# Kernel tuning notes

Measured on AMD Instinct MI355X. Metric: run time of the kernel, lower is better.

Reference implementation:

```python
import jax, jax.numpy as jnp
import numpy as np

D, DFF, H = 768, 3072, 12
HD = D // H
EPS = 1e-12

def _ln(t, gamma, beta):
    mu = t.mean(-1, keepdims=True)
    var = jnp.mean((t - mu) ** 2, -1, keepdims=True)
    return gamma * (t - mu) / jnp.sqrt(var + EPS) + beta

def setup_inputs() -> dict:
    key = jax.random.key(0)
    ks = jax.random.split(key, 16)
    s = 0.02
    x = jax.random.normal(ks[0], (2, 2048, D), jnp.float32)
    mask = jnp.ones((2, 2048), jnp.float32)
    def lin(k, out_d, in_d):
        kw, kb = jax.random.split(k)
        return (jax.random.normal(kw, (out_d, in_d), jnp.float32) * s,
                jnp.zeros((out_d,), jnp.float32))
    Wq, bq = lin(ks[1], D, D)
    Wk, bk = lin(ks[2], D, D)
    Wv, bv = lin(ks[3], D, D)
    Wp, bp = lin(ks[4], D, D)
    W1, bf1 = lin(ks[5], DFF, D)
    W2, bf2 = lin(ks[6], D, DFF)
    g1 = jnp.ones((D,), jnp.float32); be1 = jnp.zeros((D,), jnp.float32)
    g2 = jnp.ones((D,), jnp.float32); be2 = jnp.zeros((D,), jnp.float32)
    return dict(x=x, mask=mask, Wq=Wq, bq=bq, Wk=Wk, bk=bk, Wv=Wv, bv=bv,
                Wp=Wp, bp=bp, g1=g1, be1=be1, W1=W1, bf1=bf1, W2=W2, bf2=bf2,
                g2=g2, be2=be2)

def reference(x, mask, Wq, bq, Wk, bk, Wv, bv, Wp, bp, g1, be1, W1, bf1, W2, bf2, g2, be2):
    B, S, _ = x.shape
    # projections (torch Linear: x @ W^T + b)
    q = (x @ Wq.T + bq).reshape(B, S, H, HD).transpose(0, 2, 1, 3)  # [B,H,S,HD]
    k = (x @ Wk.T + bk).reshape(B, S, H, HD).transpose(0, 2, 1, 3)
    v = (x @ Wv.T + bv).reshape(B, S, H, HD).transpose(0, 2, 1, 3)
    scores = jnp.einsum('bhqd,bhkd->bhqk', q, k) / jnp.sqrt(jnp.float32(HD))
    scores = scores - 10000.0 * (1.0 - mask[:, None, None, :])
    p = jax.nn.softmax(scores, axis=-1)  # dropout is identity at eval
    h = jnp.einsum('bhqk,bhkd->bqhd', p, v).reshape(B, S, D)
    h = h @ Wp.T + bp
    x1 = _ln(x + h, g1, be1)
    ff = jax.nn.gelu(x1 @ W1.T + bf1, approximate=False) @ W2.T + bf2
    return _ln(x1 + ff, g2, be2)
```

## Files before the change

### kernel.cpp

```cpp
#include <hip/hip_runtime.h>
#include <hip/hip_bf16.h>
#include <math.h>

#define D_MODEL 768
#define D_FF    3072
#define N_HEAD  12
#define HEAD_D  64
#define BATCH   2
#define SEQ     2048
#define QKV_LD  2304

typedef __attribute__((ext_vector_type(8))) short short8;
typedef __attribute__((ext_vector_type(8))) unsigned short ushort8;
typedef __attribute__((ext_vector_type(4))) float f32x4;

__device__ inline unsigned short f2bf(float f) {
    union { __hip_bfloat16 b; unsigned short u; } cv;
    cv.b = __float2bfloat16(f);
    return cv.u;
}

__device__ inline float bf2f(unsigned short u) {
    union { unsigned int i; float f; } cv;
    cv.i = ((unsigned int)u) << 16;
    return cv.f;
}

__device__ inline void async_load16(const void* g, void* l) {
    __builtin_amdgcn_global_load_lds(
        (const __attribute__((address_space(1))) void*)g,
        (__attribute__((address_space(3))) void*)l, 16, 0, 0);
}

__global__ __launch_bounds__(256) void conv_fused(
    const float* __restrict__ x,
    const float* __restrict__ Wq, const float* __restrict__ Wk,
    const float* __restrict__ Wv, const float* __restrict__ Wp,
    const float* __restrict__ W1, const float* __restrict__ W2,
    const float* __restrict__ bq, const float* __restrict__ bk,
    const float* __restrict__ bv,
    unsigned short* __restrict__ xb, unsigned short* __restrict__ wqkvb,
    unsigned short* __restrict__ wpb, unsigned short* __restrict__ w1b,
    unsigned short* __restrict__ w2b, float* __restrict__ bqkv)
{
    int bid = blockIdx.x;
    const float* src; unsigned short* dst; int base;
    if      (bid < 3072) { src = x;  dst = xb;              base = bid;        }
    else if (bid < 3648) { src = Wq; dst = wqkvb;           base = bid - 3072; }
    else if (bid < 4224) { src = Wk; dst = wqkvb + 589824;  base = bid - 3648; }
    else if (bid < 4800) { src = Wv; dst = wqkvb + 1179648; base = bid - 4224; }
    else if (bid < 5376) { src = Wp; dst = wpb;             base = bid - 4800; }
    else if (bid < 7680) { src = W1; dst = w1b;             base = bid - 5376; }
    else if (bid < 9984) { src = W2; dst = w2b;             base = bid - 7680; }
    else {
        for (int j = threadIdx.x; j < QKV_LD; j += 256)
            bqkv[j] = (j < 768) ? bq[j] : (j < 1536) ? bk[j - 768] : bv[j - 1536];
        return;
    }
    int i = (base * 256 + threadIdx.x) * 4;
    float4 v = *(const float4*)(src + i);
    ushort4 o4;
    o4.x = f2bf(v.x); o4.y = f2bf(v.y); o4.z = f2bf(v.z); o4.w = f2bf(v.w);
    *(ushort4*)(dst + i) = o4;
}

#define NSTAGE 3

__global__ __launch_bounds__(256) void gemm_bf16(
    const unsigned short* __restrict__ A, int lda,
    const unsigned short* __restrict__ W, int ldw,
    const float* __restrict__ bias,
    const unsigned short* __restrict__ resb, int ldr,
    float* __restrict__ outf, unsigned short* __restrict__ outb,
    float* __restrict__ pacc, int ldo,
    int M, int N, int K, int mode)
{
    __shared__ unsigned short As[NSTAGE][128 * 32];
    __shared__ unsigned short Bs[NSTAGE][128 * 32];

    const int t    = threadIdx.x;
    const int lane = t & 63;
    const int wv   = t >> 6;
    const int wm   = wv >> 1;
    const int wn   = wv & 1;
    const int bm   = blockIdx.y * 128;
    const int bn   = blockIdx.x * 128;
    const int kz   = blockIdx.z;
    const int Kc   = K / gridDim.z;

    const int qd   = lane >> 4;
    const int l16  = lane & 15;

    f32x4 acc[4][4];
    #pragma unroll
    for (int i = 0; i < 4; i++)
        #pragma unroll
        for (int j = 0; j < 4; j++)
            acc[i][j] = (f32x4){0.f, 0.f, 0.f, 0.f};

    const int srow = lane >> 2;
    const int sseg = (lane & 3) * 8;
    const int r0   = (wv * 2 + 0) * 16 + srow;
    const int r1   = (wv * 2 + 1) * 16 + srow;
    const size_t gA0 = (size_t)(bm + r0) * lda + sseg;
    const size_t gA1 = (size_t)(bm + r1) * lda + sseg;
    const size_t gB0 = (size_t)(bn + r0) * ldw + sseg;
    const size_t gB1 = (size_t)(bn + r1) * ldw + sseg;
    const int c0 = (wv * 2 + 0) * 512;
    const int c1 = (wv * 2 + 1) * 512;

    const int kbeg  = kz * Kc;
    const int niter = Kc / 32;

    async_load16(A + gA0 + kbeg, &As[0][c0]);
    async_load16(W + gB0 + kbeg, &Bs[0][c0]);
    async_load16(A + gA1 + kbeg, &As[0][c1]);
    async_load16(W + gB1 + kbeg, &Bs[0][c1]);
    if (niter > 1) {
        async_load16(A + gA0 + kbeg + 32, &As[1][c0]);
        async_load16(W + gB0 + kbeg + 32, &Bs[1][c0]);
        async_load16(A + gA1 + kbeg + 32, &As[1][c1]);
        async_load16(W + gB1 + kbeg + 32, &Bs[1][c1]);
    }

    int stage = 0;
    for (int it = 0; it < niter; it++) {
        if (it + 1 < niter) __builtin_amdgcn_s_waitcnt(0x0F74);
        else                __builtin_amdgcn_s_waitcnt(0x0F70);
        __builtin_amdgcn_s_barrier();

        if (it + 2 < niter) {
            const int sn = (stage + 2 >= NSTAGE) ? stage + 2 - NSTAGE : stage + 2;
            const int kn = kbeg + (it + 2) * 32;
            async_load16(A + gA0 + kn, &As[sn][c0]);
            async_load16(W + gB0 + kn, &Bs[sn][c0]);
            async_load16(A + gA1 + kn, &As[sn][c1]);
            async_load16(W + gB1 + kn, &Bs[sn][c1]);
        }

        short8 af[4], bf[4];
        #pragma unroll
        for (int mt = 0; mt < 4; mt++)
            af[mt] = *(const short8*)(&As[stage][(wm * 64 + mt * 16 + l16) * 32 + qd * 8]);
        #pragma unroll
        for (int nt = 0; nt < 4; nt++)
            bf[nt] = *(const short8*)(&Bs[stage][(wn * 64 + nt * 16 + l16) * 32 + qd * 8]);
        #pragma unroll
        for (int mt = 0; mt < 4; mt++)
            #pragma unroll
            for (int nt = 0; nt < 4; nt++)
                acc[mt][nt] = __builtin_amdgcn_mfma_f32_16x16x32_bf16(
                    af[mt], bf[nt], acc[mt][nt], 0, 0, 0);

        stage = (stage == NSTAGE - 1) ? 0 : stage + 1;
    }

    #pragma unroll
    for (int mt = 0; mt < 4; mt++) {
        #pragma unroll
        for (int nt = 0; nt < 4; nt++) {
            int col = bn + wn * 64 + nt * 16 + l16;
            float bv = (kz == 0) ? bias[col] : 0.f;
            #pragma unroll
            for (int r = 0; r < 4; r++) {
                int row = bm + wm * 64 + mt * 16 + qd * 4 + r;
                if (kz != 0) {
                    pacc[(size_t)row * ldo + col] = acc[mt][nt][r];
                    continue;
                }
                float v = acc[mt][nt][r] + bv;
                if (mode == 1) {
                    v += bf2f(resb[(size_t)row * ldr + col]);
                    outf[(size_t)row * ldo + col] = v;
                } else if (mode == 2) {
                    v = 0.5f * v * (1.0f + erff(v * 0.70710678118654752f));
                    outb[(size_t)row * ldo + col] = f2bf(v);
                } else if (mode == 3) {
                    outb[(size_t)row * ldo + col] = f2bf(v);
                } else {
                    outf[(size_t)row * ldo + col] = v;
                }
            }
        }
    }
}

__global__ __launch_bounds__(256) void gemm_qkv(
    const unsigned short* __restrict__ A,
    const unsigned short* __restrict__ W,
    const float* __restrict__ bias,
    unsigned short* __restrict__ outb)
{
    __shared__ unsigned short As[4][128 * 32];
    __shared__ unsigned short Bs[4][128 * 32];

    const int t    = threadIdx.x;
    const int lane = t & 63;
    const int wv   = t >> 6;
    const int wm   = wv >> 1;
    const int wn   = wv & 1;

    const int flat = blockIdx.y * 18 + blockIdx.x;
    const int xcd  = flat & 7;
    const int u    = flat >> 3;
    const int mi   = (xcd >> 1) * 8 + u / 9;
    const int ni   = (xcd & 1) * 9 + u % 9;
    const int bm   = mi * 128;
    const int bn   = ni * 128;

    const int qd   = lane >> 4;
    const int l16  = lane & 15;

    f32x4 acc[4][4];
    #pragma unroll
    for (int i = 0; i < 4; i++)
        #pragma unroll
        for (int j = 0; j < 4; j++)
            acc[i][j] = (f32x4){0.f, 0.f, 0.f, 0.f};

    const int srow = lane >> 2;
    const int sseg = (lane & 3) * 8;
    const int r0   = (wv * 2 + 0) * 16 + srow;
    const int r1   = (wv * 2 + 1) * 16 + srow;
    const size_t gA0 = (size_t)(bm + r0) * D_MODEL + sseg;
    const size_t gA1 = (size_t)(bm + r1) * D_MODEL + sseg;
    const size_t gB0 = (size_t)(bn + r0) * D_MODEL + sseg;
    const size_t gB1 = (size_t)(bn + r1) * D_MODEL + sseg;
    const int c0 = (wv * 2 + 0) * 512;
    const int c1 = (wv * 2 + 1) * 512;

    const int niter = D_MODEL / 32;

    async_load16(A + gA0, &As[0][c0]);
    async_load16(W + gB0, &Bs[0][c0]);
    async_load16(A + gA1, &As[0][c1]);
    async_load16(W + gB1, &Bs[0][c1]);
    async_load16(A + gA0 + 32, &As[1][c0]);
    async_load16(W + gB0 + 32, &Bs[1][c0]);
    async_load16(A + gA1 + 32, &As[1][c1]);
    async_load16(W + gB1 + 32, &Bs[1][c1]);
    async_load16(A + gA0 + 64, &As[2][c0]);
    async_load16(W + gB0 + 64, &Bs[2][c0]);
    async_load16(A + gA1 + 64, &As[2][c1]);
    async_load16(W + gB1 + 64, &Bs[2][c1]);

    int stage = 0;
    for (int it = 0; it < niter; it++) {
        if      (it + 2 < niter) __builtin_amdgcn_s_waitcnt(0x0F78);
        else if (it + 1 < niter) __builtin_amdgcn_s_waitcnt(0x0F74);
        else                     __builtin_amdgcn_s_waitcnt(0x0F70);
        __builtin_amdgcn_s_barrier();

        if (it + 3 < niter) {
            int sn = stage + 3;
            if (sn >= 4) sn -= 4;
            const int kn = (it + 3) * 32;
            async_load16(A + gA0 + kn, &As[sn][c0]);
            async_load16(W + gB0 + kn, &Bs[sn][c0]);
            async_load16(A + gA1 + kn, &As[sn][c1]);
            async_load16(W + gB1 + kn, &Bs[sn][c1]);
        }

        short8 af[4], bf[4];
        #pragma unroll
        for (int mt = 0; mt < 4; mt++)
            af[mt] = *(const short8*)(&As[stage][(wm * 64 + mt * 16 + l16) * 32 + qd * 8]);
        #pragma unroll
        for (int nt = 0; nt < 4; nt++)
            bf[nt] = *(const short8*)(&Bs[stage][(wn * 64 + nt * 16 + l16) * 32 + qd * 8]);
        #pragma unroll
        for (int mt = 0; mt < 4; mt++)
            #pragma unroll
            for (int nt = 0; nt < 4; nt++)
                acc[mt][nt] = __builtin_amdgcn_mfma_f32_16x16x32_bf16(
                    af[mt], bf[nt], acc[mt][nt], 0, 0, 0);

        stage = (stage == 3) ? 0 : stage + 1;
    }

    #pragma unroll
    for (int mt = 0; mt < 4; mt++) {
        #pragma unroll
        for (int nt = 0; nt < 4; nt++) {
            int col = bn + wn * 64 + nt * 16 + l16;
            float bv = bias[col];
            #pragma unroll
            for (int r = 0; r < 4; r++) {
                int row = bm + wm * 64 + mt * 16 + qd * 4 + r;
                outb[(size_t)row * QKV_LD + col] = f2bf(acc[mt][nt][r] + bv);
            }
        }
    }
}

__global__ __launch_bounds__(256) void gemm_ffn1(
    const unsigned short* __restrict__ A,
    const unsigned short* __restrict__ W,
    const float* __restrict__ bias,
    unsigned short* __restrict__ outb)
{
    __shared__ unsigned short As[NSTAGE][128 * 32];
    __shared__ unsigned short Bs[NSTAGE][128 * 32];

    const int t    = threadIdx.x;
    const int lane = t & 63;
    const int wv   = t >> 6;
    const int wm   = wv >> 1;
    const int wn   = wv & 1;

    const int flat = blockIdx.y * 24 + blockIdx.x;
    const int xcd  = flat & 7;
    const int u    = flat >> 3;
    const int mi   = (xcd >> 1) * 8 + u / 12;
    const int ni   = (xcd & 1) * 12 + u % 12;
    const int bm   = mi * 128;
    const int bn   = ni * 128;

    const int qd   = lane >> 4;
    const int l16  = lane & 15;

    f32x4 acc[4][4];
    #pragma unroll
    for (int i = 0; i < 4; i++)
        #pragma unroll
        for (int j = 0; j < 4; j++)
            acc[i][j] = (f32x4){0.f, 0.f, 0.f, 0.f};

    const int srow = lane >> 2;
    const int sseg = (lane & 3) * 8;
    const int r0   = (wv * 2 + 0) * 16 + srow;
    const int r1   = (wv * 2 + 1) * 16 + srow;
    const size_t gA0 = (size_t)(bm + r0) * D_MODEL + sseg;
    const size_t gA1 = (size_t)(bm + r1) * D_MODEL + sseg;
    const size_t gB0 = (size_t)(bn + r0) * D_MODEL + sseg;
    const size_t gB1 = (size_t)(bn + r1) * D_MODEL + sseg;
    const int c0 = (wv * 2 + 0) * 512;
    const int c1 = (wv * 2 + 1) * 512;

    const int niter = D_MODEL / 32;

    async_load16(A + gA0, &As[0][c0]);
    async_load16(W + gB0, &Bs[0][c0]);
    async_load16(A + gA1, &As[0][c1]);
    async_load16(W + gB1, &Bs[0][c1]);
    async_load16(A + gA0 + 32, &As[1][c0]);
    async_load16(W + gB0 + 32, &Bs[1][c0]);
    async_load16(A + gA1 + 32, &As[1][c1]);
    async_load16(W + gB1 + 32, &Bs[1][c1]);

    int stage = 0;
    for (int it = 0; it < niter; it++) {
        if (it + 1 < niter) __builtin_amdgcn_s_waitcnt(0x0F74);
        else                __builtin_amdgcn_s_waitcnt(0x0F70);
        __builtin_amdgcn_s_barrier();

        if (it + 2 < niter) {
            const int sn = (stage + 2 >= NSTAGE) ? stage + 2 - NSTAGE : stage + 2;
            const int kn = (it + 2) * 32;
            async_load16(A + gA0 + kn, &As[sn][c0]);
            async_load16(W + gB0 + kn, &Bs[sn][c0]);
            async_load16(A + gA1 + kn, &As[sn][c1]);
            async_load16(W + gB1 + kn, &Bs[sn][c1]);
        }

        short8 af[4], bf[4];
        #pragma unroll
        for (int mt = 0; mt < 4; mt++)
            af[mt] = *(const short8*)(&As[stage][(wm * 64 + mt * 16 + l16) * 32 + qd * 8]);
        #pragma unroll
        for (int nt = 0; nt < 4; nt++)
            bf[nt] = *(const short8*)(&Bs[stage][(wn * 64 + nt * 16 + l16) * 32 + qd * 8]);
        #pragma unroll
        for (int mt = 0; mt < 4; mt++)
            #pragma unroll
            for (int nt = 0; nt < 4; nt++)
                acc[mt][nt] = __builtin_amdgcn_mfma_f32_16x16x32_bf16(
                    af[mt], bf[nt], acc[mt][nt], 0, 0, 0);

        stage = (stage == NSTAGE - 1) ? 0 : stage + 1;
    }

    #pragma unroll
    for (int mt = 0; mt < 4; mt++) {
        #pragma unroll
        for (int nt = 0; nt < 4; nt++) {
            int col = bn + wn * 64 + nt * 16 + l16;
            float bv = bias[col];
            #pragma unroll
            for (int r = 0; r < 4; r++) {
                int row = bm + wm * 64 + mt * 16 + qd * 4 + r;
                float v = acc[mt][nt][r] + bv;
                v = 0.5f * v * (1.0f + erff(v * 0.70710678118654752f));
                outb[(size_t)row * D_FF + col] = f2bf(v);
            }
        }
    }
}

__global__ __launch_bounds__(256) void gemm_ffn2(
    const unsigned short* __restrict__ A,
    const unsigned short* __restrict__ W,
    const float* __restrict__ bias,
    const unsigned short* __restrict__ resb,
    float* __restrict__ outf,
    float* __restrict__ pacc)
{
    __shared__ unsigned short As[2][128 * 64];
    __shared__ unsigned short Bs[2][128 * 64];

    const int t    = threadIdx.x;
    const int lane = t & 63;
    const int wv   = t >> 6;
    const int wm   = wv >> 1;
    const int wn   = wv & 1;

    const int flat = blockIdx.x;
    const int g    = flat & 7;
    const int u    = flat >> 3;
    const int kz   = g >> 2;
    const int g2   = g & 3;
    const int band = u / 24;
    const int rr   = (u % 24) / 6;
    const int cc   = u % 6;
    const int bm   = (g2 * 8 + band * 4 + rr) * 128;
    const int bn   = cc * 128;

    const int qd   = lane >> 4;
    const int l16  = lane & 15;

    f32x4 acc[4][4];
    #pragma unroll
    for (int i = 0; i < 4; i++)
        #pragma unroll
        for (int j = 0; j < 4; j++)
            acc[i][j] = (f32x4){0.f, 0.f, 0.f, 0.f};

    const int srow8 = lane >> 3;
    const int scol  = ((lane & 7) ^ srow8) * 8;
    const size_t gA_base = (size_t)(bm + wv * 32 + srow8) * D_FF + scol;
    const size_t gB_base = (size_t)(bn + wv * 32 + srow8) * D_FF + scol;
    const int ldsb = wv * 4 * 512;

    const int kbeg  = kz * (D_FF / 2);
    const int niter = (D_FF / 2) / 64;

    #pragma unroll
    for (int j = 0; j < 4; j++) {
        async_load16(A + gA_base + (size_t)(j * 8) * D_FF + kbeg, &As[0][ldsb + j * 512]);
        async_load16(W + gB_base + (size_t)(j * 8) * D_FF + kbeg, &Bs[0][ldsb + j * 512]);
    }

    for (int it = 0; it < niter; it++) {
        __builtin_amdgcn_s_waitcnt(0x0F70);
        __builtin_amdgcn_s_barrier();
        const int st = it & 1;

        if (it + 1 < niter) {
            const int kn = kbeg + (it + 1) * 64;
            #pragma unroll
            for (int j = 0; j < 4; j++) {
                async_load16(A + gA_base + (size_t)(j * 8) * D_FF + kn, &As[st ^ 1][ldsb + j * 512]);
                async_load16(W + gB_base + (size_t)(j * 8) * D_FF + kn, &Bs[st ^ 1][ldsb + j * 512]);
            }
        }

        #pragma unroll
        for (int kk = 0; kk < 2; kk++) {
            short8 af[4], bf[4];
            #pragma unroll
            for (int mt = 0; mt < 4; mt++) {
                const int row = wm * 64 + mt * 16 + l16;
                const int slot = (kk * 4 + qd) ^ (row & 7);
                af[mt] = *(const short8*)&As[st][row * 64 + slot * 8];
            }
            #pragma unroll
            for (int nt = 0; nt < 4; nt++) {
                const int row = wn * 64 + nt * 16 + l16;
                const int slot = (kk * 4 + qd) ^ (row & 7);
                bf[nt] = *(const short8*)&Bs[st][row * 64 + slot * 8];
            }
            #pragma unroll
            for (int mt = 0; mt < 4; mt++)
                #pragma unroll
                for (int nt = 0; nt < 4; nt++)
                    acc[mt][nt] = __builtin_amdgcn_mfma_f32_16x16x32_bf16(
                        af[mt], bf[nt], acc[mt][nt], 0, 0, 0);
        }
    }

    #pragma unroll
    for (int mt = 0; mt < 4; mt++) {
        #pragma unroll
        for (int nt = 0; nt < 4; nt++) {
            int col = bn + wn * 64 + nt * 16 + l16;
            #pragma unroll
            for (int r = 0; r < 4; r++) {
                int row = bm + wm * 64 + mt * 16 + qd * 4 + r;
                if (kz != 0) {
                    pacc[(size_t)row * D_MODEL + col] = acc[mt][nt][r];
                } else {
                    float v = acc[mt][nt][r] + bias[col]
                            + bf2f(resb[(size_t)row * D_MODEL + col]);
                    outf[(size_t)row * D_MODEL + col] = v;
                }
            }
        }
    }
}

__global__ __launch_bounds__(256) void vtrans(
    const unsigned short* __restrict__ qkv, unsigned short* __restrict__ vT)
{
    __shared__ unsigned short T[64 * 72];
    const int t   = threadIdx.x;
    const int kt  = blockIdx.x;
    const int bh  = blockIdx.y;
    const int h   = bh % N_HEAD;
    const int b   = bh / N_HEAD;
    const int row = t >> 2;
    const int c0  = (t & 3) * 16;

    const unsigned short* src =
        qkv + (size_t)(b * SEQ + kt * 64 + row) * QKV_LD + 1536 + h * HEAD_D + c0;
    *(ushort8*)&T[row * 72 + c0]     = *(const ushort8*)src;
    *(ushort8*)&T[row * 72 + c0 + 8] = *(const ushort8*)(src + 8);
    __syncthreads();

    const int d = t >> 2;
    ushort8 o0, o1;
    #pragma unroll
    for (int j = 0; j < 8; j++) o0[j] = T[(c0 + j) * 72 + d];
    #pragma unroll
    for (int j = 0; j < 8; j++) o1[j] = T[(c0 + 8 + j) * 72 + d];
    unsigned short* dst = vT + ((size_t)bh * HEAD_D + d) * SEQ + kt * 64 + c0;
    *(ushort8*)dst       = o0;
    *(ushort8*)(dst + 8) = o1;
}

#define ASTR 72
#define VSTR 136

__global__ __launch_bounds__(256) void attn_mfma(
    const unsigned short* __restrict__ qkv, const unsigned short* __restrict__ vT,
    const float* __restrict__ mask, unsigned short* __restrict__ out)
{
    __shared__ __align__(16) unsigned short Ks[128 * ASTR];
    __shared__ __align__(16) unsigned short Vt[64 * VSTR];
    __shared__ float Ms[128];

    const int t    = threadIdx.x;
    const int lane = t & 63;
    const int wv   = t >> 6;
    const int l16  = lane & 15;
    const int quad = lane >> 4;
    const int q0   = blockIdx.x * 64;
    const int bh   = blockIdx.y;
    const int h    = bh % N_HEAD;
    const int b    = bh / N_HEAD;
    const int NT   = SEQ / 128;

    const unsigned short* qb  = qkv + (size_t)b * SEQ * QKV_LD + h * HEAD_D;
    const unsigned short* kb  = qb + 768;
    const unsigned short* vtb = vT + (size_t)bh * HEAD_D * SEQ;

    {
        const int qsrow = t >> 2;
        const int qsc0  = (t & 3) * 16;
        const ushort8* src = (const ushort8*)(qb + (size_t)(q0 + qsrow) * QKV_LD + qsc0);
        *(ushort8*)&Ks[qsrow * ASTR + qsc0]     = src[0];
        *(ushort8*)&Ks[qsrow * ASTR + qsc0 + 8] = src[1];
    }
    __syncthreads();
    short8 bq0 = *(const short8*)&Ks[(wv * 16 + l16) * ASTR + quad * 8];
    short8 bq1 = *(const short8*)&Ks[(wv * 16 + l16) * ASTR + 32 + quad * 8];
    __syncthreads();

    const int krow_s = t >> 1;
    const int kc0    = (t & 1) * 32;
    const int ks6    = krow_s & 63;
    const int ksig   = (krow_s & 64) |
                       ((ks6 & 0x23) | ((ks6 & 0x04) << 2) | ((ks6 & 0x18) >> 1));
    const int vrow_s = t >> 2;
    const int vc0    = (t & 3) * 32;

    f32x4 o[4];
    #pragma unroll
    for (int i = 0; i < 4; i++) o[i] = (f32x4){0.f, 0.f, 0.f, 0.f};
    float m_st = -INFINITY, l_st = 0.f;

    ushort8 rk0, rk1, rk2, rk3, rv0, rv1, rv2, rv3;
    float rm = 1.0f;
    {
        const ushort8* ksrc = (const ushort8*)(kb + (size_t)krow_s * QKV_LD + kc0);
        rk0 = ksrc[0]; rk1 = ksrc[1]; rk2 = ksrc[2]; rk3 = ksrc[3];
        const ushort8* vsrc = (const ushort8*)(vtb + (size_t)vrow_s * SEQ + vc0);
        rv0 = vsrc[0]; rv1 = vsrc[1]; rv2 = vsrc[2]; rv3 = vsrc[3];
        if (t < 128) rm = mask[b * SEQ + t];
    }

    for (int kt = 0; kt < NT; kt++) {
        *(ushort8*)&Ks[ksig * ASTR + kc0]      = rk0;
        *(ushort8*)&Ks[ksig * ASTR + kc0 + 8]  = rk1;
        *(ushort8*)&Ks[ksig * ASTR + kc0 + 16] = rk2;
        *(ushort8*)&Ks[ksig * ASTR + kc0 + 24] = rk3;
        *(ushort8*)&Vt[vrow_s * VSTR + vc0]      = rv0;
        *(ushort8*)&Vt[vrow_s * VSTR + vc0 + 8]  = rv1;
        *(ushort8*)&Vt[vrow_s * VSTR + vc0 + 16] = rv2;
        *(ushort8*)&Vt[vrow_s * VSTR + vc0 + 24] = rv3;
        if (t < 128) Ms[t] = -10000.0f * (1.0f - rm);
        __syncthreads();

        if (kt + 1 < NT) {
            const int kn = (kt + 1) * 128;
            const ushort8* ksrc = (const ushort8*)(kb + (size_t)(kn + krow_s) * QKV_LD + kc0);
            rk0 = ksrc[0]; rk1 = ksrc[1]; rk2 = ksrc[2]; rk3 = ksrc[3];
            const ushort8* vsrc = (const ushort8*)(vtb + (size_t)vrow_s * SEQ + kn + vc0);
            rv0 = vsrc[0]; rv1 = vsrc[1]; rv2 = vsrc[2]; rv3 = vsrc[3];
            if (t < 128) rm = mask[b * SEQ + kn + t];
        }

        float p[8][4];
        float mx = -3.0e38f;
        #pragma unroll
        for (int bi = 0; bi < 8; bi++) {
            const int krow = (bi * 16 + l16) * ASTR;
            short8 k0 = *(const short8*)&Ks[krow + quad * 8];
            short8 k1 = *(const short8*)&Ks[krow + 32 + quad * 8];
            f32x4 z = (f32x4){0.f, 0.f, 0.f, 0.f};
            z = __builtin_amdgcn_mfma_f32_16x16x32_bf16(k0, bq0, z, 0, 0, 0);
            z = __builtin_amdgcn_mfma_f32_16x16x32_bf16(k1, bq1, z, 0, 0, 0);
            const float4 m4 = *(const float4*)
                &Ms[(bi >> 2) * 64 + ((bi >> 1) & 1) * 32 + quad * 8 + (bi & 1) * 4];
            #pragma unroll
            for (int r = 0; r < 4; r++) {
                float s = fmaf(z[r], 0.125f, ((const float*)&m4)[r]);
                p[bi][r] = s;
                mx = fmaxf(mx, s);
            }
        }
        mx = fmaxf(mx, __shfl_xor(mx, 16, 64));
        mx = fmaxf(mx, __shfl_xor(mx, 32, 64));
        if (__any(mx > m_st)) {
            float m_new = fmaxf(m_st, mx);
            float alpha = __expf(m_st - m_new);
            m_st = m_new;
            l_st *= alpha;
            float ar[4];
            #pragma unroll
            for (int r = 0; r < 4; r++) ar[r] = __shfl(alpha, quad * 4 + r, 64);
            #pragma unroll
            for (int nt = 0; nt < 4; nt++)
                #pragma unroll
                for (int r = 0; r < 4; r++)
                    o[nt][r] *= ar[r];
        }
        float ls = 0.f;
        #pragma unroll
        for (int bi = 0; bi < 8; bi++) {
            #pragma unroll
            for (int r = 0; r < 4; r++) {
                p[bi][r] = __expf(p[bi][r] - m_st);
                ls += p[bi][r];
            }
        }
        ls += __shfl_xor(ls, 16, 64);
        ls += __shfl_xor(ls, 32, 64);
        l_st += ls;

        short8 pf[4];
        #pragma unroll
        for (int w = 0; w < 4; w++) {
            #pragma unroll
            for (int bsel = 0; bsel < 2; bsel++) {
                #pragma unroll
                for (int r = 0; r < 4; r++)
                    pf[w][bsel * 4 + r] = (short)f2bf(p[w * 2 + bsel][r]);
            }
        }

        #pragma unroll
        for (int nt = 0; nt < 4; nt++) {
            const int vrow = (nt * 16 + l16) * VSTR;
            #pragma unroll
            for (int w = 0; w < 4; w++) {
                short8 vv = *(const short8*)&Vt[vrow + w * 32 + quad * 8];
                o[nt] = __builtin_amdgcn_mfma_f32_16x16x32_bf16(pf[w], vv, o[nt], 0, 0, 0);
            }
        }
        __syncthreads();
    }

    float inv = 1.0f / l_st;
    float ir[4];
    #pragma unroll
    for (int r = 0; r < 4; r++) ir[r] = __shfl(inv, quad * 4 + r, 64);
    #pragma unroll
    for (int nt = 0; nt < 4; nt++) {
        #pragma unroll
        for (int r = 0; r < 4; r++) {
            int qi = q0 + wv * 16 + quad * 4 + r;
            out[(size_t)(b * SEQ + qi) * D_MODEL + h * HEAD_D + nt * 16 + l16] =
                f2bf(o[nt][r] * ir[r]);
        }
    }
}

__global__ __launch_bounds__(256) void ln_kernel(
    const float* __restrict__ in, const float* __restrict__ in2,
    const float* __restrict__ g, const float* __restrict__ be,
    float* __restrict__ outf, unsigned short* __restrict__ outb)
{
    const int row = blockIdx.x;
    const int t   = threadIdx.x;
    const float* rp  = in  + (size_t)row * D_MODEL;
    const float* rp2 = in2 ? in2 + (size_t)row * D_MODEL : nullptr;

    float vals[3];
    float s = 0.f, s2 = 0.f;
    #pragma unroll
    for (int i = 0; i < 3; i++) {
        float x = rp[t + i * 256];
        if (rp2) x += rp2[t + i * 256];
        vals[i] = x;
        s += x; s2 += x * x;
    }
    #pragma unroll
    for (int off = 32; off >= 1; off >>= 1) {
        s  += __shfl_xor(s,  off, 64);
        s2 += __shfl_xor(s2, off, 64);
    }
    __shared__ float rs[4], rs2[4];
    __shared__ float mu_s, rstd_s;
    const int wave = t >> 6, lane = t & 63;
    if (lane == 0) { rs[wave] = s; rs2[wave] = s2; }
    __syncthreads();
    if (t == 0) {
        float S1 = rs[0] + rs[1] + rs[2] + rs[3];
        float S2 = rs2[0] + rs2[1] + rs2[2] + rs2[3];
        float mu  = S1 * (1.0f / D_MODEL);
        float var = S2 * (1.0f / D_MODEL) - mu * mu;
        mu_s = mu;
        rstd_s = rsqrtf(var + 1e-12f);
    }
    __syncthreads();
    const float mu = mu_s, rstd = rstd_s;
    #pragma unroll
    for (int i = 0; i < 3; i++) {
        int c = t + i * 256;
        float o = g[c] * (vals[i] - mu) * rstd + be[c];
        if (outf) outf[(size_t)row * D_MODEL + c] = o;
        if (outb) outb[(size_t)row * D_MODEL + c] = f2bf(o);
    }
}

extern "C" void kernel_launch(void* const* d_in, const int* in_sizes, int n_in,
                              void* d_out, int out_size, void* d_ws, size_t ws_size,
                              hipStream_t stream)
{
    const float* x    = (const float*)d_in[0];
    const float* mask = (const float*)d_in[1];
    const float* Wq   = (const float*)d_in[2];
    const float* bq   = (const float*)d_in[3];
    const float* Wk   = (const float*)d_in[4];
    const float* bk   = (const float*)d_in[5];
    const float* Wv   = (const float*)d_in[6];
    const float* bv   = (const float*)d_in[7];
    const float* Wp   = (const float*)d_in[8];
    const float* bp   = (const float*)d_in[9];
    const float* g1   = (const float*)d_in[10];
    const float* be1  = (const float*)d_in[11];
    const float* W1   = (const float*)d_in[12];
    const float* bf1  = (const float*)d_in[13];
    const float* W2   = (const float*)d_in[14];
    const float* bf2  = (const float*)d_in[15];
    const float* g2   = (const float*)d_in[16];
    const float* be2  = (const float*)d_in[17];

    const int M = BATCH * SEQ;

    char* ws = (char*)d_ws;
    unsigned short* qkvb  = (unsigned short*)(ws + 0);
    unsigned short* ff1b  = (unsigned short*)(ws + 0);
    unsigned short* xb    = (unsigned short*)(ws + 25165824);
    unsigned short* hb    = (unsigned short*)(ws + 31457280);
    unsigned short* x1b   = (unsigned short*)(ws + 31457280);
    float*          y0    = (float*)(ws + 37748736);
    unsigned short* wqkvb = (unsigned short*)(ws + 50331648);
    unsigned short* wpb   = (unsigned short*)(ws + 53870592);
    unsigned short* w1b   = (unsigned short*)(ws + 55050240);
    unsigned short* w2b   = (unsigned short*)(ws + 59768832);
    float*          bqkv  = (float*)(ws + 64487424);
    float*          p1    = (float*)(ws + 64496640);
    unsigned short* vTb   = (unsigned short*)(ws + 77079552);

    dim3 blk(256);

    conv_fused<<<dim3(9985), blk, 0, stream>>>(
        x, Wq, Wk, Wv, Wp, W1, W2, bq, bk, bv,
        xb, wqkvb, wpb, w1b, w2b, bqkv);

    gemm_qkv<<<dim3(QKV_LD / 128, M / 128), blk, 0, stream>>>(xb, wqkvb, bqkv, qkvb);

    vtrans<<<dim3(SEQ / 64, BATCH * N_HEAD), blk, 0, stream>>>(qkvb, vTb);

    attn_mfma<<<dim3(SEQ / 64, BATCH * N_HEAD), blk, 0, stream>>>(qkvb, vTb, mask, hb);

    gemm_bf16<<<dim3(D_MODEL / 128, M / 128, 2), blk, 0, stream>>>(
        hb, D_MODEL, wpb, D_MODEL, bp, xb, D_MODEL,
        y0, nullptr, p1, D_MODEL, M, D_MODEL, D_MODEL, 1);

    ln_kernel<<<dim3(M), blk, 0, stream>>>(y0, p1, g1, be1, nullptr, x1b);

    gemm_ffn1<<<dim3(D_FF / 128, M / 128), blk, 0, stream>>>(x1b, w1b, bf1, ff1b);

    gemm_ffn2<<<dim3(384), blk, 0, stream>>>(ff1b, w2b, bf2, x1b, y0, p1);

    ln_kernel<<<dim3(M), blk, 0, stream>>>(y0, p1, g2, be2, (float*)d_out, nullptr);
}
```

Baseline: 334.3 us.

## Split attention over two key/value halves and merge partial softmax results

The attention kernel now runs a grid dimension of 2. Each block processes half of the key/value sequence and writes unnormalized fp32 partial outputs along with its running max and sum. A new merge kernel rescales the two partials by their log-sum-exp weights, normalizes, and writes the bf16 head output. This doubles the number of attention blocks to improve occupancy and latency hiding, at the cost of extra fp32 partial traffic and an additional kernel launch.

```diff
diff --git a/kernel.cpp b/kernel.cpp
--- a/kernel.cpp
+++ b/kernel.cpp
@@ -542,7 +542,8 @@
 
 __global__ __launch_bounds__(256) void attn_mfma(
     const unsigned short* __restrict__ qkv, const unsigned short* __restrict__ vT,
-    const float* __restrict__ mask, unsigned short* __restrict__ out)
+    const float* __restrict__ mask,
+    float* __restrict__ o0p, float* __restrict__ o1p, float* __restrict__ mlbuf)
 {
     __shared__ __align__(16) unsigned short Ks[128 * ASTR];
     __shared__ __align__(16) unsigned short Vt[64 * VSTR];
@@ -555,9 +556,11 @@
     const int quad = lane >> 4;
     const int q0   = blockIdx.x * 64;
     const int bh   = blockIdx.y;
+    const int z    = blockIdx.z;
     const int h    = bh % N_HEAD;
     const int b    = bh / N_HEAD;
-    const int NT   = SEQ / 128;
+    const int kt0  = z * 8;
+    const int ktE  = kt0 + 8;
 
     const unsigned short* qb  = qkv + (size_t)b * SEQ * QKV_LD + h * HEAD_D;
     const unsigned short* kb  = qb + 768;
@@ -591,14 +594,14 @@
     ushort8 rk0, rk1, rk2, rk3, rv0, rv1, rv2, rv3;
     float rm = 1.0f;
     {
-        const ushort8* ksrc = (const ushort8*)(kb + (size_t)krow_s * QKV_LD + kc0);
+        const ushort8* ksrc = (const ushort8*)(kb + (size_t)(kt0 * 128 + krow_s) * QKV_LD + kc0);
         rk0 = ksrc[0]; rk1 = ksrc[1]; rk2 = ksrc[2]; rk3 = ksrc[3];
-        const ushort8* vsrc = (const ushort8*)(vtb + (size_t)vrow_s * SEQ + vc0);
+        const ushort8* vsrc = (const ushort8*)(vtb + (size_t)vrow_s * SEQ + kt0 * 128 + vc0);
         rv0 = vsrc[0]; rv1 = vsrc[1]; rv2 = vsrc[2]; rv3 = vsrc[3];
-        if (t < 128) rm = mask[b * SEQ + t];
-    }
-
-    for (int kt = 0; kt < NT; kt++) {
+        if (t < 128) rm = mask[b * SEQ + kt0 * 128 + t];
+    }
+
+    for (int kt = kt0; kt < ktE; kt++) {
         *(ushort8*)&Ks[ksig * ASTR + kc0]      = rk0;
         *(ushort8*)&Ks[ksig * ASTR + kc0 + 8]  = rk1;
         *(ushort8*)&Ks[ksig * ASTR + kc0 + 16] = rk2;
@@ -610,7 +613,7 @@
         if (t < 128) Ms[t] = -10000.0f * (1.0f - rm);
         __syncthreads();
 
-        if (kt + 1 < NT) {
+        if (kt + 1 < ktE) {
             const int kn = (kt + 1) * 128;
             const ushort8* ksrc = (const ushort8*)(kb + (size_t)(kn + krow_s) * QKV_LD + kc0);
             rk0 = ksrc[0]; rk1 = ksrc[1]; rk2 = ksrc[2]; rk3 = ksrc[3];
@@ -626,14 +629,14 @@
             const int krow = (bi * 16 + l16) * ASTR;
             short8 k0 = *(const short8*)&Ks[krow + quad * 8];
             short8 k1 = *(const short8*)&Ks[krow + 32 + quad * 8];
-            f32x4 z = (f32x4){0.f, 0.f, 0.f, 0.f};
-            z = __builtin_amdgcn_mfma_f32_16x16x32_bf16(k0, bq0, z, 0, 0, 0);
-            z = __builtin_amdgcn_mfma_f32_16x16x32_bf16(k1, bq1, z, 0, 0, 0);
+            f32x4 zf = (f32x4){0.f, 0.f, 0.f, 0.f};
+            zf = __builtin_amdgcn_mfma_f32_16x16x32_bf16(k0, bq0, zf, 0, 0, 0);
+            zf = __builtin_amdgcn_mfma_f32_16x16x32_bf16(k1, bq1, zf, 0, 0, 0);
             const float4 m4 = *(const float4*)
                 &Ms[(bi >> 2) * 64 + ((bi >> 1) & 1) * 32 + quad * 8 + (bi & 1) * 4];
             #pragma unroll
             for (int r = 0; r < 4; r++) {
-                float s = fmaf(z[r], 0.125f, ((const float*)&m4)[r]);
+                float s = fmaf(zf[r], 0.125f, ((const float*)&m4)[r]);
                 p[bi][r] = s;
                 mx = fmaxf(mx, s);
             }
@@ -683,26 +686,55 @@
             const int vrow = (nt * 16 + l16) * VSTR;
             #pragma unroll
             for (int w = 0; w < 4; w++) {
-                short8 vv = *(const short8*)&Vt[vrow + w * 32 + quad * 8];
-                o[nt] = __builtin_amdgcn_mfma_f32_16x16x32_bf16(pf[w], vv, o[nt], 0, 0, 0);
+                short8 vvf = *(const short8*)&Vt[vrow + w * 32 + quad * 8];
+                o[nt] = __builtin_amdgcn_mfma_f32_16x16x32_bf16(pf[w], vvf, o[nt], 0, 0, 0);
             }
         }
         __syncthreads();
     }
 
-    float inv = 1.0f / l_st;
-    float ir[4];
-    #pragma unroll
-    for (int r = 0; r < 4; r++) ir[r] = __shfl(inv, quad * 4 + r, 64);
+    float* opart = (z == 0) ? o0p : o1p;
     #pragma unroll
     for (int nt = 0; nt < 4; nt++) {
         #pragma unroll
         for (int r = 0; r < 4; r++) {
             int qi = q0 + wv * 16 + quad * 4 + r;
-            out[(size_t)(b * SEQ + qi) * D_MODEL + h * HEAD_D + nt * 16 + l16] =
-                f2bf(o[nt][r] * ir[r]);
-        }
-    }
+            opart[((size_t)bh * SEQ + qi) * HEAD_D + nt * 16 + l16] = o[nt][r];
+        }
+    }
+    if (lane < 16) {
+        int q = q0 + wv * 16 + lane;
+        mlbuf[(z * 24 + bh) * SEQ + q]         = m_st;
+        mlbuf[98304 + (z * 24 + bh) * SEQ + q] = l_st;
+    }
+}
+
+__global__ __launch_bounds__(256) void attn_merge(
+    const float* __restrict__ o0p, const float* __restrict__ o1p,
+    const float* __restrict__ mlbuf, unsigned short* __restrict__ out)
+{
+    const int idx = blockIdx.x * 256 + threadIdx.x;
+    const int row = idx >> 4;
+    const int dq  = (idx & 15) * 4;
+    const int bh  = row >> 11, q = row & 2047;
+    const int b   = bh / N_HEAD, h = bh % N_HEAD;
+
+    const float m0 = mlbuf[row];
+    const float m1 = mlbuf[49152 + row];
+    const float l0 = mlbuf[98304 + row];
+    const float l1 = mlbuf[98304 + 49152 + row];
+    const float mx = fmaxf(m0, m1);
+    const float w0 = __expf(m0 - mx), w1 = __expf(m1 - mx);
+    const float inv = 1.0f / (l0 * w0 + l1 * w1);
+
+    const float4 a = *(const float4*)(o0p + (size_t)row * HEAD_D + dq);
+    const float4 c = *(const float4*)(o1p + (size_t)row * HEAD_D + dq);
+    ushort4 r4;
+    r4.x = f2bf((a.x * w0 + c.x * w1) * inv);
+    r4.y = f2bf((a.y * w0 + c.y * w1) * inv);
+    r4.z = f2bf((a.z * w0 + c.z * w1) * inv);
+    r4.w = f2bf((a.w * w0 + c.w * w1) * inv);
+    *(ushort4*)(out + ((size_t)(b * SEQ + q)) * D_MODEL + h * HEAD_D + dq) = r4;
 }
 
 __global__ __launch_bounds__(256) void ln_kernel(
@@ -792,6 +824,7 @@
     float*          bqkv  = (float*)(ws + 64487424);
     float*          p1    = (float*)(ws + 64496640);
     unsigned short* vTb   = (unsigned short*)(ws + 77079552);
+    float*          mlbuf = (float*)(ws + 50331648);
 
     dim3 blk(256);
 
@@ -803,7 +836,10 @@
 
     vtrans<<<dim3(SEQ / 64, BATCH * N_HEAD), blk, 0, stream>>>(qkvb, vTb);
 
-    attn_mfma<<<dim3(SEQ / 64, BATCH * N_HEAD), blk, 0, stream>>>(qkvb, vTb, mask, hb);
+    attn_mfma<<<dim3(SEQ / 64, BATCH * N_HEAD, 2), blk, 0, stream>>>(
+        qkvb, vTb, mask, y0, p1, mlbuf);
+
+    attn_merge<<<dim3(6144), blk, 0, stream>>>(y0, p1, mlbuf, hb);
 
     gemm_bf16<<<dim3(D_MODEL / 128, M / 128, 2), blk, 0, stream>>>(
         hb, D_MODEL, wpb, D_MODEL, bp, xb, D_MODEL,
```

New measurement: 344.5 us. 3.0% more time.
